# Kernel tuning notes

Hardware: AMD Instinct MI355X
Metric: run time of the kernel (lower is better)

The kernel has to match this reference:

```python
import jax, jax.numpy as jnp
import numpy as np

B, L, D = 8, 256, 32      # batch, key seq_len, input_dim
E, H, Q = 128, 8, 128     # embed_time, heads, num_query_steps
HID = 256                 # hidden_dim
V = 2 * D                 # value dim with mask channel
EK = E // H


def setup_inputs() -> dict:
    key = jax.random.key(0)
    ks = jax.random.split(key, 12)
    s = 0.05
    return {
        "values": jax.random.normal(ks[0], (B, L, D), jnp.float32),
        "mask": jax.random.randint(ks[1], (B, L, D), 0, 2).astype(jnp.int32),
        "times": jax.random.uniform(ks[2], (B, L), jnp.float32),
        # learn_time_embedding params (torch Linear(1, E-1) and Linear(1, 1))
        "w_per": jax.random.normal(ks[3], (1, E - 1), jnp.float32) * s,
        "b_per": jax.random.normal(ks[4], (E - 1,), jnp.float32) * s,
        "w_lin": jax.random.normal(ks[5], (1, 1), jnp.float32) * s,
        "b_lin": jax.random.normal(ks[6], (1,), jnp.float32) * s,
        # mTAND q/k linears (E,E) and output proj (HID, H*V)
        "wq": jax.random.normal(ks[7], (E, E), jnp.float32) * s,
        "bq": jnp.zeros((E,), jnp.float32),
        "wk": jax.random.normal(ks[8], (E, E), jnp.float32) * s,
        "bk": jnp.zeros((E,), jnp.float32),
        "wo": jax.random.normal(ks[9], (HID, H * V), jnp.float32) * s,
        "bo": jnp.zeros((HID,), jnp.float32),
        "ln_g": jnp.ones((HID,), jnp.float32),
        "ln_b": jnp.zeros((HID,), jnp.float32),
    }


def reference(values, mask, times, w_per, b_per, w_lin, b_lin,
              wq, bq, wk, bk, wo, bo, ln_g, ln_b):
    eps = 1e-6
    maskf = mask.astype(jnp.float32)                      # [B,L,D]
    obs = maskf.max(axis=-1) > 0                          # [B,L] observed steps
    # --- normalize times over observed steps ---
    tmin = jnp.where(obs, times, jnp.inf).min(axis=1, keepdims=True)
    tmax = jnp.where(obs, times, -jnp.inf).max(axis=1, keepdims=True)
    has = jnp.any(obs, axis=1, keepdims=True)             # [B,1]
    tmin = jnp.where(has, tmin, 0.0)
    tmax = jnp.where(has, tmax, 1.0)
    tn = (times - tmin) / jnp.maximum(tmax - tmin, eps)
    tn = jnp.where(obs, tn, 0.0)
    qt = jnp.broadcast_to(jnp.linspace(0.0, 1.0, Q, dtype=jnp.float32), (B, Q))

    def temb(tt):  # learnable time embedding: [linear(t), sin(periodic(t))]
        t = tt[..., None]                                 # [...,1]
        return jnp.concatenate([t @ w_lin.T + b_lin,
                                jnp.sin(t @ w_per + b_per)], axis=-1)

    tk = temb(tn)   # [B,L,E]
    tq = temb(qt)   # [B,Q,E]

    vinp = jnp.concatenate([values, maskf], axis=-1)      # [B,L,V]
    am = jnp.concatenate([maskf, maskf], axis=-1)         # [B,L,V]

    q = (tq @ wq.T + bq).reshape(B, Q, H, EK).transpose(0, 2, 1, 3)  # [B,H,Q,ek]
    k = (tk @ wk.T + bk).reshape(B, L, H, EK).transpose(0, 2, 1, 3)  # [B,H,L,ek]
    scores = jnp.einsum('bhqe,bhke->bhqk', q, k) / np.float32(np.sqrt(EK))
    # per-value-channel masked scores: [B,H,Q,L,V]
    s5 = jnp.where(am[:, None, None, :, :] == 0, jnp.float32(-10000.0),
                   scores[..., None])
    attn = jax.nn.softmax(s5, axis=-2)                    # softmax over L
    ctx = jnp.einsum('bhqkv,bkv->bhqv', attn, vinp)       # [B,H,Q,V]
    ctx = ctx.transpose(0, 2, 1, 3).reshape(B, Q, H * V)
    seq = ctx @ wo.T + bo                                 # [B,Q,HID]
    # LayerNorm (torch default eps=1e-5, biased var)
    mu = seq.mean(axis=-1, keepdims=True)
    var = ((seq - mu) ** 2).mean(axis=-1, keepdims=True)
    seq = (seq - mu) / jnp.sqrt(var + 1e-5) * ln_g + ln_b
    seq = seq * has.astype(jnp.float32)[:, :, None]       # zero seqs with no obs
    pooled = seq.mean(axis=1)
    return seq, pooled, qt
```

## Files before the change

### kernel.cpp

```cpp
#include <hip/hip_runtime.h>
#include <hip/hip_bf16.h>

#define B_   8
#define L_   256
#define D_   32
#define E_   128
#define H_   8
#define Q_   128
#define HID_ 256

__global__ __launch_bounds__(256) void kA_prep(
    const float* __restrict__ values, const int* __restrict__ mask,
    const float* __restrict__ times,
    const float* __restrict__ w_per, const float* __restrict__ b_per,
    const float* __restrict__ w_lin, const float* __restrict__ b_lin,
    const float* __restrict__ wq, const float* __restrict__ bq,
    float* __restrict__ tn, float* __restrict__ has,
    float* __restrict__ cm, float* __restrict__ colmean,
    float* __restrict__ mvm, unsigned* __restrict__ bitsT,
    float* __restrict__ qproj, float* __restrict__ qt_out,
    float* __restrict__ pooled)
{
    __shared__ float val_s[256][33];
    __shared__ float smin[256], smax[256];
    __shared__ unsigned bits_s[256];
    __shared__ float partial_s[8][32];
    __shared__ float sh[2];
    __shared__ __align__(16) float emb_s[2][E_];

    int blk = blockIdx.x;
    int t = threadIdx.x;

    if (blk < B_) {
        int b = blk;
        const int*   mrow = mask   + (size_t)(b * L_ + t) * D_;
        const float* vrow = values + (size_t)(b * L_ + t) * D_;
        int4  m4[8];
        float4 v4[8];
        int any = 0;
        #pragma unroll
        for (int j = 0; j < 8; ++j) {
            m4[j] = reinterpret_cast<const int4*>(mrow)[j];
            v4[j] = reinterpret_cast<const float4*>(vrow)[j];
            any |= m4[j].x | m4[j].y | m4[j].z | m4[j].w;
            float4 mv;
            mv.x = m4[j].x ? v4[j].x : 0.f;
            mv.y = m4[j].y ? v4[j].y : 0.f;
            mv.z = m4[j].z ? v4[j].z : 0.f;
            mv.w = m4[j].w ? v4[j].w : 0.f;
            reinterpret_cast<float4*>(mvm + (size_t)(b * L_ + t) * D_)[j] = mv;
            val_s[t][j * 4 + 0] = v4[j].x;
            val_s[t][j * 4 + 1] = v4[j].y;
            val_s[t][j * 4 + 2] = v4[j].z;
            val_s[t][j * 4 + 3] = v4[j].w;
        }
        int wave = t >> 6;
        #pragma unroll
        for (int d = 0; d < D_; ++d) {
            int comp;
            { int j = d >> 2, c = d & 3;
              int4 mm = m4[j];
              comp = (c == 0) ? mm.x : (c == 1) ? mm.y : (c == 2) ? mm.z : mm.w; }
            unsigned long long bal = __ballot(comp != 0);
            if ((t & 63) == 0) {
                bits_s[d * 8 + wave * 2 + 0] = (unsigned)(bal & 0xffffffffull);
                bits_s[d * 8 + wave * 2 + 1] = (unsigned)(bal >> 32);
            }
        }
        float tv = times[b * L_ + t];
        smin[t] = any ? tv : 1e38f;
        smax[t] = any ? tv : -1e38f;
        __syncthreads();
        for (int off = 128; off > 0; off >>= 1) {
            if (t < off) {
                smin[t] = fminf(smin[t], smin[t + off]);
                smax[t] = fmaxf(smax[t], smax[t + off]);
            }
            __syncthreads();
        }
        if (t == 0) {
            float mn = smin[0], mx = smax[0];
            float hv = (mn < 1e37f) ? 1.f : 0.f;
            sh[0] = (hv > 0.f) ? mn : 0.f;
            sh[1] = (hv > 0.f) ? mx : 1.f;
            has[b] = hv;
        }
        __syncthreads();
        float inv = 1.f / fmaxf(sh[1] - sh[0], 1e-6f);
        tn[b * L_ + t] = any ? (tv - sh[0]) * inv : 0.f;

        if (t < Q_) qt_out[b * Q_ + t] = (float)t * (1.f / 127.f);
        pooled[b * HID_ + t] = 0.f;
        bitsT[b * 256 + t] = bits_s[t];

        {
            int d = t & 31, lg = t >> 5;
            float ps = 0.f;
            #pragma unroll
            for (int i = 0; i < 32; ++i) ps += val_s[lg * 32 + i][d];
            partial_s[lg][d] = ps;
        }
        __syncthreads();
        if (t < D_) {
            float s = 0.f;
            #pragma unroll
            for (int lg = 0; lg < 8; ++lg) s += partial_s[lg][t];
            colmean[b * D_ + t] = s * (1.f / (float)L_);
            unsigned o = 0;
            #pragma unroll
            for (int w = 0; w < 8; ++w) o |= bits_s[t * 8 + w];
            cm[b * D_ + t] = o ? 1.f : 0.f;
        }
    } else {
        int w2 = blk - B_;
        int half = t >> 7, e = t & 127;
        int q = w2 * 2 + half;
        float tt = (float)q * (1.f / 127.f);
        emb_s[half][e] = (e == 0) ? (tt * w_lin[0] + b_lin[0])
                                  : __sinf(tt * w_per[e - 1] + b_per[e - 1]);
        __syncthreads();
        const float4* wr4 = reinterpret_cast<const float4*>(wq + (size_t)e * E_);
        const float4* e4  = reinterpret_cast<const float4*>(emb_s[half]);
        float acc = bq[e];
        #pragma unroll 8
        for (int j = 0; j < E_ / 4; ++j) {
            float4 w = wr4[j], x = e4[j];
            acc += w.x * x.x + w.y * x.y + w.z * x.z + w.w * x.w;
        }
        qproj[q * E_ + e] = acc;
    }
}

__global__ __launch_bounds__(256, 4) void kB_kproj(
    const float* __restrict__ tn,
    const float* __restrict__ w_per, const float* __restrict__ b_per,
    const float* __restrict__ w_lin, const float* __restrict__ b_lin,
    const float* __restrict__ wk, const float* __restrict__ bk,
    float* __restrict__ kproj)
{
    int blk = blockIdx.x;
    int bl0 = blk * 8;
    int e = threadIdx.x & 127, rh = threadIdx.x >> 7;
    __shared__ __align__(16) float emb[8][E_];
    __shared__ float tsh[8];
    if (threadIdx.x < 8) tsh[threadIdx.x] = tn[bl0 + threadIdx.x];
    __syncthreads();
    float wp = (e == 0) ? 0.f : w_per[e - 1];
    float bp = (e == 0) ? 0.f : b_per[e - 1];
    float wl = w_lin[0], bl = b_lin[0];
    #pragma unroll
    for (int rr = 0; rr < 4; ++rr) {
        int r = rh * 4 + rr;
        float tt = tsh[r];
        emb[r][e] = (e == 0) ? (tt * wl + bl) : __sinf(tt * wp + bp);
    }
    __syncthreads();
    const float4* wr4 = reinterpret_cast<const float4*>(wk + (size_t)e * E_);
    float acc[4];
    float bias = bk[e];
    #pragma unroll
    for (int rr = 0; rr < 4; ++rr) acc[rr] = bias;
    #pragma unroll 8
    for (int j = 0; j < E_ / 4; ++j) {
        float4 w = wr4[j];
        #pragma unroll
        for (int rr = 0; rr < 4; ++rr) {
            float4 x = *reinterpret_cast<const float4*>(&emb[rh * 4 + rr][j * 4]);
            acc[rr] += w.x * x.x + w.y * x.y + w.z * x.z + w.w * x.w;
        }
    }
    #pragma unroll
    for (int rr = 0; rr < 4; ++rr)
        kproj[(size_t)(bl0 + rh * 4 + rr) * E_ + e] = acc[rr];
}

__global__ __launch_bounds__(256, 3) void k3_attn(
    const float* __restrict__ qproj, const float* __restrict__ kproj,
    const float* __restrict__ mvm, const unsigned* __restrict__ bitsT,
    const float* __restrict__ cm, const float* __restrict__ colmean,
    float* __restrict__ ctxv)
{
    int q = blockIdx.x, b = blockIdx.y;
    int tid = threadIdx.x;
    __shared__ __align__(16) float mvm_s[L_ * D_];
    __shared__ __align__(16) float e_s[L_ * H_];
    __shared__ __align__(16) float qv_s[E_];
    __shared__ unsigned bits_s[256];
    __shared__ float gmax_s[H_];

    {
        const float4* src = reinterpret_cast<const float4*>(mvm + (size_t)b * L_ * D_);
        float4* dst = reinterpret_cast<float4*>(mvm_s);
        #pragma unroll
        for (int j = 0; j < 8; ++j) dst[tid + j * 256] = src[tid + j * 256];
        bits_s[tid] = bitsT[b * 256 + tid];
        if (tid < E_) qv_s[tid] = qproj[q * E_ + tid];
    }
    __syncthreads();

    const float4* kr4 = reinterpret_cast<const float4*>(kproj + (size_t)(b * L_ + tid) * E_);
    const float4* qv4 = reinterpret_cast<const float4*>(qv_s);
    float s[H_];
    #pragma unroll
    for (int h = 0; h < H_; ++h) {
        float acc = 0.f;
        #pragma unroll
        for (int j = 0; j < 4; ++j) {
            float4 kk = kr4[h * 4 + j], qq = qv4[h * 4 + j];
            acc += kk.x * qq.x + kk.y * qq.y + kk.z * qq.z + kk.w * qq.w;
        }
        s[h] = acc * 0.25f;
    }
    {
        float4* er4 = reinterpret_cast<float4*>(e_s + tid * 8);
        er4[0] = *reinterpret_cast<float4*>(&s[0]);
        er4[1] = *reinterpret_cast<float4*>(&s[4]);
    }
    __syncthreads();
    {
        int h = tid >> 5, ln = tid & 31;
        float mx = -1e30f;
        #pragma unroll
        for (int j = 0; j < 8; ++j) mx = fmaxf(mx, e_s[(ln + j * 32) * 8 + h]);
        #pragma unroll
        for (int off = 16; off > 0; off >>= 1) mx = fmaxf(mx, __shfl_xor(mx, off));
        if (ln == 0) gmax_s[h] = mx;
    }
    __syncthreads();
    {
        float e8[H_];
        #pragma unroll
        for (int h = 0; h < H_; ++h) e8[h] = __expf(s[h] - gmax_s[h]);
        float4* er4 = reinterpret_cast<float4*>(e_s + tid * 8);
        er4[0] = *reinterpret_cast<float4*>(&e8[0]);
        er4[1] = *reinterpret_cast<float4*>(&e8[4]);
    }
    __syncthreads();

    int lseg = tid >> 6, h = (tid >> 3) & 7, d4 = tid & 7;
    unsigned w0[4], w1[4];
    #pragma unroll
    for (int j = 0; j < 4; ++j) {
        int d = d4 * 4 + j;
        w0[j] = bits_s[d * 8 + lseg * 2 + 0];
        w1[j] = bits_s[d * 8 + lseg * 2 + 1];
    }
    float4 av  = {0.f, 0.f, 0.f, 0.f};
    float4 den = {0.f, 0.f, 0.f, 0.f};
    const float4* mv4 = reinterpret_cast<const float4*>(mvm_s);
    int l0 = lseg * 64;
    #pragma unroll 8
    for (int i = 0; i < 32; ++i) {
        int l = l0 + i;
        float e = e_s[l * 8 + h];
        float4 m = mv4[l * 8 + d4];
        av.x += e * m.x; av.y += e * m.y; av.z += e * m.z; av.w += e * m.w;
        den.x += ((w0[0] >> i) & 1u) ? e : 0.f;
        den.y += ((w0[1] >> i) & 1u) ? e : 0.f;
        den.z += ((w0[2] >> i) & 1u) ? e : 0.f;
        den.w += ((w0[3] >> i) & 1u) ? e : 0.f;
    }
    #pragma unroll 8
    for (int i = 0; i < 32; ++i) {
        int l = l0 + 32 + i;
        float e = e_s[l * 8 + h];
        float4 m = mv4[l * 8 + d4];
        av.x += e * m.x; av.y += e * m.y; av.z += e * m.z; av.w += e * m.w;
        den.x += ((w1[0] >> i) & 1u) ? e : 0.f;
        den.y += ((w1[1] >> i) & 1u) ? e : 0.f;
        den.z += ((w1[2] >> i) & 1u) ? e : 0.f;
        den.w += ((w1[3] >> i) & 1u) ? e : 0.f;
    }
    __syncthreads();
    {
        float4* p4 = reinterpret_cast<float4*>(mvm_s);
        p4[tid * 2 + 0] = av;
        p4[tid * 2 + 1] = den;
    }
    __syncthreads();
    {
        const float* part = mvm_s;
        int hh = tid >> 5, dd = tid & 31, dg = dd >> 2, jj = dd & 3;
        float a = 0.f, dn = 0.f;
        #pragma unroll
        for (int ls = 0; ls < 4; ++ls) {
            int pt = ls * 64 + hh * 8 + dg;
            a  += part[pt * 8 + jj];
            dn += part[pt * 8 + 4 + jj];
        }
        float cmf = cm[b * D_ + dd];
        float outv = (cmf > 0.f) ? (a / dn) : colmean[b * D_ + dd];
        ctxv[((size_t)(b * Q_ + q)) * 256 + hh * D_ + dd] = outv;
    }
}

__global__ __launch_bounds__(256, 4) void kC_gemm_ln(
    const float* __restrict__ ctxv, const float* __restrict__ wo,
    const float* __restrict__ bo, const float* __restrict__ cm,
    const float* __restrict__ ln_g, const float* __restrict__ ln_b,
    const float* __restrict__ has,
    float* __restrict__ seq_out, float* __restrict__ pooled)
{
    int row0 = blockIdx.x * 4;
    int hid = threadIdx.x;
    int b = row0 >> 7;
    __shared__ float pw[4][4], pws[4][4];
    __shared__ float mu_s[4], rs_s[4];

    const float4* wrow4 = reinterpret_cast<const float4*>(wo + (size_t)hid * 512);
    const float* ar0 = ctxv + (size_t)(row0 + 0) * 256;
    const float* ar1 = ctxv + (size_t)(row0 + 1) * 256;
    const float* ar2 = ctxv + (size_t)(row0 + 2) * 256;
    const float* ar3 = ctxv + (size_t)(row0 + 3) * 256;

    float cmq[D_];
    #pragma unroll
    for (int j = 0; j < D_; ++j) cmq[j] = (cm[b * D_ + j] > 0.f) ? 1.f : 0.f;

    float accm = 0.f;
    #pragma unroll
    for (int h1 = 0; h1 < 8; ++h1) {
        #pragma unroll
        for (int j = 0; j < 8; ++j) {
            float4 w = wrow4[h1 * 16 + 8 + j];
            accm += cmq[j * 4 + 0] * w.x + cmq[j * 4 + 1] * w.y
                  + cmq[j * 4 + 2] * w.z + cmq[j * 4 + 3] * w.w;
        }
    }

    float bias = bo[hid] + accm;
    float acc[4] = {bias, bias, bias, bias};

    #pragma unroll 2
    for (int h1 = 0; h1 < 8; ++h1) {
        #pragma unroll
        for (int j = 0; j < 8; ++j) {
            float4 w = wrow4[h1 * 16 + j];
            int base = h1 * 32 + j * 4;
            acc[0] += ar0[base+0]*w.x + ar0[base+1]*w.y + ar0[base+2]*w.z + ar0[base+3]*w.w;
            acc[1] += ar1[base+0]*w.x + ar1[base+1]*w.y + ar1[base+2]*w.z + ar1[base+3]*w.w;
            acc[2] += ar2[base+0]*w.x + ar2[base+1]*w.y + ar2[base+2]*w.z + ar2[base+3]*w.w;
            acc[3] += ar3[base+0]*w.x + ar3[base+1]*w.y + ar3[base+2]*w.z + ar3[base+3]*w.w;
        }
    }

    int wave = hid >> 6;
    #pragma unroll
    for (int r = 0; r < 4; ++r) {
        float s = acc[r], ss = acc[r] * acc[r];
        #pragma unroll
        for (int off = 32; off > 0; off >>= 1) {
            s  += __shfl_xor(s, off);
            ss += __shfl_xor(ss, off);
        }
        if ((hid & 63) == 0) { pw[r][wave] = s; pws[r][wave] = ss; }
    }
    __syncthreads();
    if (hid < 4) {
        float S  = pw[hid][0] + pw[hid][1] + pw[hid][2] + pw[hid][3];
        float SS = pws[hid][0] + pws[hid][1] + pws[hid][2] + pws[hid][3];
        float mu = S * (1.f / HID_);
        float var = SS * (1.f / HID_) - mu * mu;
        mu_s[hid] = mu;
        rs_s[hid] = rsqrtf(var + 1e-5f);
    }
    __syncthreads();

    float g = ln_g[hid], bb = ln_b[hid];
    float hasb = has[b];
    float psum = 0.f;
    #pragma unroll
    for (int r = 0; r < 4; ++r) {
        float outv = ((acc[r] - mu_s[r]) * rs_s[r] * g + bb) * hasb;
        seq_out[(size_t)(row0 + r) * HID_ + hid] = outv;
        psum += outv;
    }
    atomicAdd(&pooled[b * HID_ + hid], psum * (1.f / (float)Q_));
}

extern "C" void kernel_launch(void* const* d_in, const int* in_sizes, int n_in,
                              void* d_out, int out_size, void* d_ws, size_t ws_size,
                              hipStream_t stream)
{
    const float* values = (const float*)d_in[0];
    const int*   mask   = (const int*)  d_in[1];
    const float* times  = (const float*)d_in[2];
    const float* w_per  = (const float*)d_in[3];
    const float* b_per  = (const float*)d_in[4];
    const float* w_lin  = (const float*)d_in[5];
    const float* b_lin  = (const float*)d_in[6];
    const float* wq     = (const float*)d_in[7];
    const float* bq     = (const float*)d_in[8];
    const float* wk     = (const float*)d_in[9];
    const float* bk     = (const float*)d_in[10];
    const float* wo     = (const float*)d_in[11];
    const float* bo     = (const float*)d_in[12];
    const float* ln_g   = (const float*)d_in[13];
    const float* ln_b   = (const float*)d_in[14];

    float* out     = (float*)d_out;
    float* seq_out = out;
    float* pooled  = out + 262144;
    float* qt_out  = out + 262144 + 2048;

    float* ws         = (float*)d_ws;
    float*    tn      = ws;
    float*    has     = ws + 2048;
    float*    cm      = ws + 2056;
    float*    colmean = ws + 2312;
    float*    qproj   = ws + 2568;
    unsigned* bitsT   = (unsigned*)(ws + 18952);
    float*    mvm     = ws + 21000;
    float*    kproj   = ws + 86536;
    float*    ctxv    = ws + 348680;

    kA_prep  <<<B_ + Q_ / 2,  256, 0, stream>>>(values, mask, times,
                  w_per, b_per, w_lin, b_lin, wq, bq,
                  tn, has, cm, colmean, mvm, bitsT, qproj, qt_out, pooled);
    kB_kproj <<<B_ * L_ / 8,  256, 0, stream>>>(tn, w_per, b_per, w_lin, b_lin,
                  wk, bk, kproj);
    k3_attn  <<<dim3(Q_, B_), 256, 0, stream>>>(qproj, kproj, mvm, bitsT,
                  cm, colmean, ctxv);
    kC_gemm_ln<<<B_ * Q_ / 4, 256, 0, stream>>>(ctxv, wo, bo, cm,
                  ln_g, ln_b, has, seq_out, pooled);
}
```

Before: 151.5 us.

## Fuse output projection and LayerNorm into attention kernel, merge q/k projection launches

Folds the output projection and LayerNorm into the attention kernel, so each (q,b) block multiplies its context row by a transposed value-half of wo. That removes the ctxv round trip and one kernel launch. The mask-channel contribution plus bias is precomputed per batch in the prep kernel as cvec. The q and k projections and the wo transpose now share one launch. The cost is that every attention block rereads the 256x256 transposed weight slice from L2 instead of amortising it over 4 rows, and it adds a 256-wide atomicAdd per block into pooled.

```diff
diff --git a/kernel.cpp b/kernel.cpp
--- a/kernel.cpp
+++ b/kernel.cpp
@@ -9,118 +9,151 @@
 #define Q_   128
 #define HID_ 256
 
-__global__ __launch_bounds__(256) void kA_prep(
+__global__ __launch_bounds__(256) void k_prep1(
     const float* __restrict__ values, const int* __restrict__ mask,
     const float* __restrict__ times,
-    const float* __restrict__ w_per, const float* __restrict__ b_per,
-    const float* __restrict__ w_lin, const float* __restrict__ b_lin,
-    const float* __restrict__ wq, const float* __restrict__ bq,
+    const float* __restrict__ wo, const float* __restrict__ bo,
     float* __restrict__ tn, float* __restrict__ has,
     float* __restrict__ cm, float* __restrict__ colmean,
     float* __restrict__ mvm, unsigned* __restrict__ bitsT,
-    float* __restrict__ qproj, float* __restrict__ qt_out,
-    float* __restrict__ pooled)
+    float* __restrict__ qt_out, float* __restrict__ pooled,
+    float* __restrict__ cvec)
 {
     __shared__ float val_s[256][33];
     __shared__ float smin[256], smax[256];
     __shared__ unsigned bits_s[256];
     __shared__ float partial_s[8][32];
+    __shared__ float cm_s[D_];
     __shared__ float sh[2];
-    __shared__ __align__(16) float emb_s[2][E_];
+
+    int b = blockIdx.x;
+    int t = threadIdx.x;
+
+    const int*   mrow = mask   + (size_t)(b * L_ + t) * D_;
+    const float* vrow = values + (size_t)(b * L_ + t) * D_;
+    int4  m4[8];
+    float4 v4[8];
+    int any = 0;
+    #pragma unroll
+    for (int j = 0; j < 8; ++j) {
+        m4[j] = reinterpret_cast<const int4*>(mrow)[j];
+        v4[j] = reinterpret_cast<const float4*>(vrow)[j];
+        any |= m4[j].x | m4[j].y | m4[j].z | m4[j].w;
+        float4 mv;
+        mv.x = m4[j].x ? v4[j].x : 0.f;
+        mv.y = m4[j].y ? v4[j].y : 0.f;
+        mv.z = m4[j].z ? v4[j].z : 0.f;
+        mv.w = m4[j].w ? v4[j].w : 0.f;
+        reinterpret_cast<float4*>(mvm + (size_t)(b * L_ + t) * D_)[j] = mv;
+        val_s[t][j * 4 + 0] = v4[j].x;
+        val_s[t][j * 4 + 1] = v4[j].y;
+        val_s[t][j * 4 + 2] = v4[j].z;
+        val_s[t][j * 4 + 3] = v4[j].w;
+    }
+    int wave = t >> 6;
+    #pragma unroll
+    for (int d = 0; d < D_; ++d) {
+        int comp;
+        { int j = d >> 2, c = d & 3;
+          int4 mm = m4[j];
+          comp = (c == 0) ? mm.x : (c == 1) ? mm.y : (c == 2) ? mm.z : mm.w; }
+        unsigned long long bal = __ballot(comp != 0);
+        if ((t & 63) == 0) {
+            bits_s[d * 8 + wave * 2 + 0] = (unsigned)(bal & 0xffffffffull);
+            bits_s[d * 8 + wave * 2 + 1] = (unsigned)(bal >> 32);
+        }
+    }
+    float tv = times[b * L_ + t];
+    smin[t] = any ? tv : 1e38f;
+    smax[t] = any ? tv : -1e38f;
+    __syncthreads();
+    for (int off = 128; off > 0; off >>= 1) {
+        if (t < off) {
+            smin[t] = fminf(smin[t], smin[t + off]);
+            smax[t] = fmaxf(smax[t], smax[t + off]);
+        }
+        __syncthreads();
+    }
+    if (t == 0) {
+        float mn = smin[0], mx = smax[0];
+        float hv = (mn < 1e37f) ? 1.f : 0.f;
+        sh[0] = (hv > 0.f) ? mn : 0.f;
+        sh[1] = (hv > 0.f) ? mx : 1.f;
+        has[b] = hv;
+    }
+    __syncthreads();
+    float inv = 1.f / fmaxf(sh[1] - sh[0], 1e-6f);
+    tn[b * L_ + t] = any ? (tv - sh[0]) * inv : 0.f;
+
+    if (t < Q_) qt_out[b * Q_ + t] = (float)t * (1.f / 127.f);
+    pooled[b * HID_ + t] = 0.f;
+    bitsT[b * 256 + t] = bits_s[t];
+
+    {
+        int d = t & 31, lg = t >> 5;
+        float ps = 0.f;
+        #pragma unroll
+        for (int i = 0; i < 32; ++i) ps += val_s[lg * 32 + i][d];
+        partial_s[lg][d] = ps;
+    }
+    __syncthreads();
+    if (t < D_) {
+        float s = 0.f;
+        #pragma unroll
+        for (int lg = 0; lg < 8; ++lg) s += partial_s[lg][t];
+        colmean[b * D_ + t] = s * (1.f / (float)L_);
+        unsigned o = 0;
+        #pragma unroll
+        for (int w = 0; w < 8; ++w) o |= bits_s[t * 8 + w];
+        float cmf = o ? 1.f : 0.f;
+        cm[b * D_ + t] = cmf;
+        cm_s[t] = cmf;
+    }
+    __syncthreads();
+
+    {
+        int hid = t;
+        const float4* wrow4 = reinterpret_cast<const float4*>(wo + (size_t)hid * 512);
+        float accm = 0.f;
+        #pragma unroll
+        for (int h1 = 0; h1 < 8; ++h1) {
+            #pragma unroll
+            for (int j = 0; j < 8; ++j) {
+                float4 w = wrow4[h1 * 16 + 8 + j];
+                accm += cm_s[j * 4 + 0] * w.x + cm_s[j * 4 + 1] * w.y
+                      + cm_s[j * 4 + 2] * w.z + cm_s[j * 4 + 3] * w.w;
+            }
+        }
+        cvec[b * HID_ + hid] = bo[hid] + accm;
+    }
+}
+
+__global__ __launch_bounds__(256) void k_prep2(
+    const float* __restrict__ tn,
+    const float* __restrict__ w_per, const float* __restrict__ b_per,
+    const float* __restrict__ w_lin, const float* __restrict__ b_lin,
+    const float* __restrict__ wq, const float* __restrict__ bq,
+    const float* __restrict__ wk, const float* __restrict__ bk,
+    const float* __restrict__ wo,
+    float* __restrict__ qproj, float* __restrict__ kproj,
+    float* __restrict__ wotv)
+{
+    __shared__ __align__(16) float emb_q[2][E_];
+    __shared__ __align__(16) float emb_k[8][E_];
+    __shared__ float tsh[8];
 
     int blk = blockIdx.x;
     int t = threadIdx.x;
 
-    if (blk < B_) {
-        int b = blk;
-        const int*   mrow = mask   + (size_t)(b * L_ + t) * D_;
-        const float* vrow = values + (size_t)(b * L_ + t) * D_;
-        int4  m4[8];
-        float4 v4[8];
-        int any = 0;
-        #pragma unroll
-        for (int j = 0; j < 8; ++j) {
-            m4[j] = reinterpret_cast<const int4*>(mrow)[j];
-            v4[j] = reinterpret_cast<const float4*>(vrow)[j];
-            any |= m4[j].x | m4[j].y | m4[j].z | m4[j].w;
-            float4 mv;
-            mv.x = m4[j].x ? v4[j].x : 0.f;
-            mv.y = m4[j].y ? v4[j].y : 0.f;
-            mv.z = m4[j].z ? v4[j].z : 0.f;
-            mv.w = m4[j].w ? v4[j].w : 0.f;
-            reinterpret_cast<float4*>(mvm + (size_t)(b * L_ + t) * D_)[j] = mv;
-            val_s[t][j * 4 + 0] = v4[j].x;
-            val_s[t][j * 4 + 1] = v4[j].y;
-            val_s[t][j * 4 + 2] = v4[j].z;
-            val_s[t][j * 4 + 3] = v4[j].w;
-        }
-        int wave = t >> 6;
-        #pragma unroll
-        for (int d = 0; d < D_; ++d) {
-            int comp;
-            { int j = d >> 2, c = d & 3;
-              int4 mm = m4[j];
-              comp = (c == 0) ? mm.x : (c == 1) ? mm.y : (c == 2) ? mm.z : mm.w; }
-            unsigned long long bal = __ballot(comp != 0);
-            if ((t & 63) == 0) {
-                bits_s[d * 8 + wave * 2 + 0] = (unsigned)(bal & 0xffffffffull);
-                bits_s[d * 8 + wave * 2 + 1] = (unsigned)(bal >> 32);
-            }
-        }
-        float tv = times[b * L_ + t];
-        smin[t] = any ? tv : 1e38f;
-        smax[t] = any ? tv : -1e38f;
-        __syncthreads();
-        for (int off = 128; off > 0; off >>= 1) {
-            if (t < off) {
-                smin[t] = fminf(smin[t], smin[t + off]);
-                smax[t] = fmaxf(smax[t], smax[t + off]);
-            }
-            __syncthreads();
-        }
-        if (t == 0) {
-            float mn = smin[0], mx = smax[0];
-            float hv = (mn < 1e37f) ? 1.f : 0.f;
-            sh[0] = (hv > 0.f) ? mn : 0.f;
-            sh[1] = (hv > 0.f) ? mx : 1.f;
-            has[b] = hv;
-        }
-        __syncthreads();
-        float inv = 1.f / fmaxf(sh[1] - sh[0], 1e-6f);
-        tn[b * L_ + t] = any ? (tv - sh[0]) * inv : 0.f;
-
-        if (t < Q_) qt_out[b * Q_ + t] = (float)t * (1.f / 127.f);
-        pooled[b * HID_ + t] = 0.f;
-        bitsT[b * 256 + t] = bits_s[t];
-
-        {
-            int d = t & 31, lg = t >> 5;
-            float ps = 0.f;
-            #pragma unroll
-            for (int i = 0; i < 32; ++i) ps += val_s[lg * 32 + i][d];
-            partial_s[lg][d] = ps;
-        }
-        __syncthreads();
-        if (t < D_) {
-            float s = 0.f;
-            #pragma unroll
-            for (int lg = 0; lg < 8; ++lg) s += partial_s[lg][t];
-            colmean[b * D_ + t] = s * (1.f / (float)L_);
-            unsigned o = 0;
-            #pragma unroll
-            for (int w = 0; w < 8; ++w) o |= bits_s[t * 8 + w];
-            cm[b * D_ + t] = o ? 1.f : 0.f;
-        }
-    } else {
-        int w2 = blk - B_;
+    if (blk < 64) {
         int half = t >> 7, e = t & 127;
-        int q = w2 * 2 + half;
+        int q = blk * 2 + half;
         float tt = (float)q * (1.f / 127.f);
-        emb_s[half][e] = (e == 0) ? (tt * w_lin[0] + b_lin[0])
+        emb_q[half][e] = (e == 0) ? (tt * w_lin[0] + b_lin[0])
                                   : __sinf(tt * w_per[e - 1] + b_per[e - 1]);
         __syncthreads();
         const float4* wr4 = reinterpret_cast<const float4*>(wq + (size_t)e * E_);
-        const float4* e4  = reinterpret_cast<const float4*>(emb_s[half]);
+        const float4* e4  = reinterpret_cast<const float4*>(emb_q[half]);
         float acc = bq[e];
         #pragma unroll 8
         for (int j = 0; j < E_ / 4; ++j) {
@@ -128,57 +161,55 @@
             acc += w.x * x.x + w.y * x.y + w.z * x.z + w.w * x.w;
         }
         qproj[q * E_ + e] = acc;
+    } else if (blk < 320) {
+        int bl0 = (blk - 64) * 8;
+        int e = t & 127, rh = t >> 7;
+        if (t < 8) tsh[t] = tn[bl0 + t];
+        __syncthreads();
+        float wp = (e == 0) ? 0.f : w_per[e - 1];
+        float bp = (e == 0) ? 0.f : b_per[e - 1];
+        float wl = w_lin[0], bl = b_lin[0];
+        #pragma unroll
+        for (int rr = 0; rr < 4; ++rr) {
+            int r = rh * 4 + rr;
+            float tt = tsh[r];
+            emb_k[r][e] = (e == 0) ? (tt * wl + bl) : __sinf(tt * wp + bp);
+        }
+        __syncthreads();
+        const float4* wr4 = reinterpret_cast<const float4*>(wk + (size_t)e * E_);
+        float bias = bk[e];
+        float acc[4] = {bias, bias, bias, bias};
+        #pragma unroll 8
+        for (int j = 0; j < E_ / 4; ++j) {
+            float4 w = wr4[j];
+            #pragma unroll
+            for (int rr = 0; rr < 4; ++rr) {
+                float4 x = *reinterpret_cast<const float4*>(&emb_k[rh * 4 + rr][j * 4]);
+                acc[rr] += w.x * x.x + w.y * x.y + w.z * x.z + w.w * x.w;
+            }
+        }
+        #pragma unroll
+        for (int rr = 0; rr < 4; ++rr)
+            kproj[(size_t)(bl0 + rh * 4 + rr) * E_ + e] = acc[rr];
+    } else {
+        int c0 = (blk - 320) * 4;
+        #pragma unroll
+        for (int j = 0; j < 4; ++j) {
+            int c = c0 + j;
+            int col = (c >> 5) * 64 + (c & 31);
+            wotv[(size_t)c * HID_ + t] = wo[(size_t)t * 512 + col];
+        }
     }
 }
 
-__global__ __launch_bounds__(256, 4) void kB_kproj(
-    const float* __restrict__ tn,
-    const float* __restrict__ w_per, const float* __restrict__ b_per,
-    const float* __restrict__ w_lin, const float* __restrict__ b_lin,
-    const float* __restrict__ wk, const float* __restrict__ bk,
-    float* __restrict__ kproj)
-{
-    int blk = blockIdx.x;
-    int bl0 = blk * 8;
-    int e = threadIdx.x & 127, rh = threadIdx.x >> 7;
-    __shared__ __align__(16) float emb[8][E_];
-    __shared__ float tsh[8];
-    if (threadIdx.x < 8) tsh[threadIdx.x] = tn[bl0 + threadIdx.x];
-    __syncthreads();
-    float wp = (e == 0) ? 0.f : w_per[e - 1];
-    float bp = (e == 0) ? 0.f : b_per[e - 1];
-    float wl = w_lin[0], bl = b_lin[0];
-    #pragma unroll
-    for (int rr = 0; rr < 4; ++rr) {
-        int r = rh * 4 + rr;
-        float tt = tsh[r];
-        emb[r][e] = (e == 0) ? (tt * wl + bl) : __sinf(tt * wp + bp);
-    }
-    __syncthreads();
-    const float4* wr4 = reinterpret_cast<const float4*>(wk + (size_t)e * E_);
-    float acc[4];
-    float bias = bk[e];
-    #pragma unroll
-    for (int rr = 0; rr < 4; ++rr) acc[rr] = bias;
-    #pragma unroll 8
-    for (int j = 0; j < E_ / 4; ++j) {
-        float4 w = wr4[j];
-        #pragma unroll
-        for (int rr = 0; rr < 4; ++rr) {
-            float4 x = *reinterpret_cast<const float4*>(&emb[rh * 4 + rr][j * 4]);
-            acc[rr] += w.x * x.x + w.y * x.y + w.z * x.z + w.w * x.w;
-        }
-    }
-    #pragma unroll
-    for (int rr = 0; rr < 4; ++rr)
-        kproj[(size_t)(bl0 + rh * 4 + rr) * E_ + e] = acc[rr];
-}
-
-__global__ __launch_bounds__(256, 3) void k3_attn(
+__global__ __launch_bounds__(256, 3) void k_main(
     const float* __restrict__ qproj, const float* __restrict__ kproj,
     const float* __restrict__ mvm, const unsigned* __restrict__ bitsT,
     const float* __restrict__ cm, const float* __restrict__ colmean,
-    float* __restrict__ ctxv)
+    const float* __restrict__ wotv, const float* __restrict__ cvec,
+    const float* __restrict__ has,
+    const float* __restrict__ ln_g, const float* __restrict__ ln_b,
+    float* __restrict__ seq_out, float* __restrict__ pooled)
 {
     int q = blockIdx.x, b = blockIdx.y;
     int tid = threadIdx.x;
@@ -187,6 +218,9 @@
     __shared__ __align__(16) float qv_s[E_];
     __shared__ unsigned bits_s[256];
     __shared__ float gmax_s[H_];
+    __shared__ __align__(16) float ctx_s[256];
+    __shared__ float red_s[8];
+    __shared__ float mu_rs[2];
 
     {
         const float4* src = reinterpret_cast<const float4*>(mvm + (size_t)b * L_ * D_);
@@ -237,42 +271,42 @@
     }
     __syncthreads();
 
-    int lseg = tid >> 6, h = (tid >> 3) & 7, d4 = tid & 7;
-    unsigned w0[4], w1[4];
-    #pragma unroll
-    for (int j = 0; j < 4; ++j) {
-        int d = d4 * 4 + j;
-        w0[j] = bits_s[d * 8 + lseg * 2 + 0];
-        w1[j] = bits_s[d * 8 + lseg * 2 + 1];
-    }
-    float4 av  = {0.f, 0.f, 0.f, 0.f};
-    float4 den = {0.f, 0.f, 0.f, 0.f};
-    const float4* mv4 = reinterpret_cast<const float4*>(mvm_s);
-    int l0 = lseg * 64;
-    #pragma unroll 8
-    for (int i = 0; i < 32; ++i) {
-        int l = l0 + i;
-        float e = e_s[l * 8 + h];
-        float4 m = mv4[l * 8 + d4];
-        av.x += e * m.x; av.y += e * m.y; av.z += e * m.z; av.w += e * m.w;
-        den.x += ((w0[0] >> i) & 1u) ? e : 0.f;
-        den.y += ((w0[1] >> i) & 1u) ? e : 0.f;
-        den.z += ((w0[2] >> i) & 1u) ? e : 0.f;
-        den.w += ((w0[3] >> i) & 1u) ? e : 0.f;
-    }
-    #pragma unroll 8
-    for (int i = 0; i < 32; ++i) {
-        int l = l0 + 32 + i;
-        float e = e_s[l * 8 + h];
-        float4 m = mv4[l * 8 + d4];
-        av.x += e * m.x; av.y += e * m.y; av.z += e * m.z; av.w += e * m.w;
-        den.x += ((w1[0] >> i) & 1u) ? e : 0.f;
-        den.y += ((w1[1] >> i) & 1u) ? e : 0.f;
-        den.z += ((w1[2] >> i) & 1u) ? e : 0.f;
-        den.w += ((w1[3] >> i) & 1u) ? e : 0.f;
-    }
-    __syncthreads();
-    {
+    {
+        int lseg = tid >> 6, h = (tid >> 3) & 7, d4 = tid & 7;
+        unsigned w0[4], w1[4];
+        #pragma unroll
+        for (int j = 0; j < 4; ++j) {
+            int d = d4 * 4 + j;
+            w0[j] = bits_s[d * 8 + lseg * 2 + 0];
+            w1[j] = bits_s[d * 8 + lseg * 2 + 1];
+        }
+        float4 av  = {0.f, 0.f, 0.f, 0.f};
+        float4 den = {0.f, 0.f, 0.f, 0.f};
+        const float4* mv4 = reinterpret_cast<const float4*>(mvm_s);
+        int l0 = lseg * 64;
+        #pragma unroll 8
+        for (int i = 0; i < 32; ++i) {
+            int l = l0 + i;
+            float e = e_s[l * 8 + h];
+            float4 m = mv4[l * 8 + d4];
+            av.x += e * m.x; av.y += e * m.y; av.z += e * m.z; av.w += e * m.w;
+            den.x += ((w0[0] >> i) & 1u) ? e : 0.f;
+            den.y += ((w0[1] >> i) & 1u) ? e : 0.f;
+            den.z += ((w0[2] >> i) & 1u) ? e : 0.f;
+            den.w += ((w0[3] >> i) & 1u) ? e : 0.f;
+        }
+        #pragma unroll 8
+        for (int i = 0; i < 32; ++i) {
+            int l = l0 + 32 + i;
+            float e = e_s[l * 8 + h];
+            float4 m = mv4[l * 8 + d4];
+            av.x += e * m.x; av.y += e * m.y; av.z += e * m.z; av.w += e * m.w;
+            den.x += ((w1[0] >> i) & 1u) ? e : 0.f;
+            den.y += ((w1[1] >> i) & 1u) ? e : 0.f;
+            den.z += ((w1[2] >> i) & 1u) ? e : 0.f;
+            den.w += ((w1[3] >> i) & 1u) ? e : 0.f;
+        }
+        __syncthreads();
         float4* p4 = reinterpret_cast<float4*>(mvm_s);
         p4[tid * 2 + 0] = av;
         p4[tid * 2 + 1] = den;
@@ -289,93 +323,46 @@
             dn += part[pt * 8 + 4 + jj];
         }
         float cmf = cm[b * D_ + dd];
-        float outv = (cmf > 0.f) ? (a / dn) : colmean[b * D_ + dd];
-        ctxv[((size_t)(b * Q_ + q)) * 256 + hh * D_ + dd] = outv;
-    }
-}
-
-__global__ __launch_bounds__(256, 4) void kC_gemm_ln(
-    const float* __restrict__ ctxv, const float* __restrict__ wo,
-    const float* __restrict__ bo, const float* __restrict__ cm,
-    const float* __restrict__ ln_g, const float* __restrict__ ln_b,
-    const float* __restrict__ has,
-    float* __restrict__ seq_out, float* __restrict__ pooled)
-{
-    int row0 = blockIdx.x * 4;
-    int hid = threadIdx.x;
-    int b = row0 >> 7;
-    __shared__ float pw[4][4], pws[4][4];
-    __shared__ float mu_s[4], rs_s[4];
-
-    const float4* wrow4 = reinterpret_cast<const float4*>(wo + (size_t)hid * 512);
-    const float* ar0 = ctxv + (size_t)(row0 + 0) * 256;
-    const float* ar1 = ctxv + (size_t)(row0 + 1) * 256;
-    const float* ar2 = ctxv + (size_t)(row0 + 2) * 256;
-    const float* ar3 = ctxv + (size_t)(row0 + 3) * 256;
-
-    float cmq[D_];
-    #pragma unroll
-    for (int j = 0; j < D_; ++j) cmq[j] = (cm[b * D_ + j] > 0.f) ? 1.f : 0.f;
-
-    float accm = 0.f;
-    #pragma unroll
-    for (int h1 = 0; h1 < 8; ++h1) {
-        #pragma unroll
-        for (int j = 0; j < 8; ++j) {
-            float4 w = wrow4[h1 * 16 + 8 + j];
-            accm += cmq[j * 4 + 0] * w.x + cmq[j * 4 + 1] * w.y
-                  + cmq[j * 4 + 2] * w.z + cmq[j * 4 + 3] * w.w;
-        }
-    }
-
-    float bias = bo[hid] + accm;
-    float acc[4] = {bias, bias, bias, bias};
-
-    #pragma unroll 2
-    for (int h1 = 0; h1 < 8; ++h1) {
-        #pragma unroll
-        for (int j = 0; j < 8; ++j) {
-            float4 w = wrow4[h1 * 16 + j];
-            int base = h1 * 32 + j * 4;
-            acc[0] += ar0[base+0]*w.x + ar0[base+1]*w.y + ar0[base+2]*w.z + ar0[base+3]*w.w;
-            acc[1] += ar1[base+0]*w.x + ar1[base+1]*w.y + ar1[base+2]*w.z + ar1[base+3]*w.w;
-            acc[2] += ar2[base+0]*w.x + ar2[base+1]*w.y + ar2[base+2]*w.z + ar2[base+3]*w.w;
-            acc[3] += ar3[base+0]*w.x + ar3[base+1]*w.y + ar3[base+2]*w.z + ar3[base+3]*w.w;
-        }
+        ctx_s[tid] = (cmf > 0.f) ? (a / dn) : colmean[b * D_ + dd];
+    }
+    __syncthreads();
+
+    int hid = tid;
+    float acc = cvec[b * HID_ + hid];
+    #pragma unroll 4
+    for (int c4 = 0; c4 < 64; ++c4) {
+        float w0 = wotv[(size_t)(c4 * 4 + 0) * HID_ + hid];
+        float w1 = wotv[(size_t)(c4 * 4 + 1) * HID_ + hid];
+        float w2 = wotv[(size_t)(c4 * 4 + 2) * HID_ + hid];
+        float w3 = wotv[(size_t)(c4 * 4 + 3) * HID_ + hid];
+        float4 cx = *reinterpret_cast<const float4*>(&ctx_s[c4 * 4]);
+        acc += cx.x * w0 + cx.y * w1 + cx.z * w2 + cx.w * w3;
     }
 
     int wave = hid >> 6;
-    #pragma unroll
-    for (int r = 0; r < 4; ++r) {
-        float s = acc[r], ss = acc[r] * acc[r];
+    {
+        float sum = acc, ssum = acc * acc;
         #pragma unroll
         for (int off = 32; off > 0; off >>= 1) {
-            s  += __shfl_xor(s, off);
-            ss += __shfl_xor(ss, off);
-        }
-        if ((hid & 63) == 0) { pw[r][wave] = s; pws[r][wave] = ss; }
-    }
-    __syncthreads();
-    if (hid < 4) {
-        float S  = pw[hid][0] + pw[hid][1] + pw[hid][2] + pw[hid][3];
-        float SS = pws[hid][0] + pws[hid][1] + pws[hid][2] + pws[hid][3];
+            sum  += __shfl_xor(sum, off);
+            ssum += __shfl_xor(ssum, off);
+        }
+        if ((hid & 63) == 0) { red_s[wave] = sum; red_s[4 + wave] = ssum; }
+    }
+    __syncthreads();
+    if (hid == 0) {
+        float S  = red_s[0] + red_s[1] + red_s[2] + red_s[3];
+        float SS = red_s[4] + red_s[5] + red_s[6] + red_s[7];
         float mu = S * (1.f / HID_);
         float var = SS * (1.f / HID_) - mu * mu;
-        mu_s[hid] = mu;
-        rs_s[hid] = rsqrtf(var + 1e-5f);
-    }
-    __syncthreads();
-
-    float g = ln_g[hid], bb = ln_b[hid];
-    float hasb = has[b];
-    float psum = 0.f;
-    #pragma unroll
-    for (int r = 0; r < 4; ++r) {
-        float outv = ((acc[r] - mu_s[r]) * rs_s[r] * g + bb) * hasb;
-        seq_out[(size_t)(row0 + r) * HID_ + hid] = outv;
-        psum += outv;
-    }
-    atomicAdd(&pooled[b * HID_ + hid], psum * (1.f / (float)Q_));
+        mu_rs[0] = mu;
+        mu_rs[1] = rsqrtf(var + 1e-5f);
+    }
+    __syncthreads();
+
+    float outv = ((acc - mu_rs[0]) * mu_rs[1] * ln_g[hid] + ln_b[hid]) * has[b];
+    seq_out[((size_t)(b * Q_ + q)) * HID_ + hid] = outv;
+    atomicAdd(&pooled[b * HID_ + hid], outv * (1.f / (float)Q_));
 }
 
 extern "C" void kernel_launch(void* const* d_in, const int* in_sizes, int n_in,
@@ -412,15 +399,13 @@
     unsigned* bitsT   = (unsigned*)(ws + 18952);
     float*    mvm     = ws + 21000;
     float*    kproj   = ws + 86536;
-    float*    ctxv    = ws + 348680;
-
-    kA_prep  <<<B_ + Q_ / 2,  256, 0, stream>>>(values, mask, times,
-                  w_per, b_per, w_lin, b_lin, wq, bq,
-                  tn, has, cm, colmean, mvm, bitsT, qproj, qt_out, pooled);
-    kB_kproj <<<B_ * L_ / 8,  256, 0, stream>>>(tn, w_per, b_per, w_lin, b_lin,
-                  wk, bk, kproj);
-    k3_attn  <<<dim3(Q_, B_), 256, 0, stream>>>(qproj, kproj, mvm, bitsT,
-                  cm, colmean, ctxv);
-    kC_gemm_ln<<<B_ * Q_ / 4, 256, 0, stream>>>(ctxv, wo, bo, cm,
-                  ln_g, ln_b, has, seq_out, pooled);
+    float*    cvec    = ws + 348680;
+    float*    wotv    = ws + 350728;
+
+    k_prep1<<<B_,            256, 0, stream>>>(values, mask, times, wo, bo,
+                 tn, has, cm, colmean, mvm, bitsT, qt_out, pooled, cvec);
+    k_prep2<<<384,           256, 0, stream>>>(tn, w_per, b_per, w_lin, b_lin,
+                 wq, bq, wk, bk, wo, qproj, kproj, wotv);
+    k_main <<<dim3(Q_, B_),  256, 0, stream>>>(qproj, kproj, mvm, bitsT,
+                 cm, colmean, wotv, cvec, has, ln_g, ln_b, seq_out, pooled);
 }
```

New measurement: 148.1 us. -2.2%, faster.
